# Optimization experiments

Measured on AMD Instinct MI355X. Metric: run time of the kernel, lower is better.

Reference implementation:

```python
import jax, jax.numpy as jnp
import numpy as np

N_NODES = 100000


def _gcn_conv(x, row, col, W, b, n):
    # PyG GCNConv: h = W x; out_i = sum_{j->i} norm_ij * h_j + b, with self-loops
    # and symmetric normalization norm_ij = deg_i^-1/2 * deg_j^-1/2.
    h = x @ W  # [N, out]
    loop = jnp.arange(n, dtype=row.dtype)
    r = jnp.concatenate([row, loop])
    c = jnp.concatenate([col, loop])
    deg = jax.ops.segment_sum(jnp.ones_like(c, dtype=h.dtype), c, num_segments=n)
    dinv = jnp.where(deg > 0, jax.lax.rsqrt(deg), 0.0)
    norm = dinv[r] * dinv[c]  # [E+N]
    msg = h[r] * norm[:, None]  # gather + per-edge scale
    out = jax.ops.segment_sum(msg, c, num_segments=n)  # scatter-add to dst
    return out + b


def setup_inputs() -> dict:
    key = jax.random.key(0)
    ks = jax.random.split(key, 8)
    N, E = N_NODES, 1600000
    d_in, comm_dim, hid, out = 120, 8, 128, 64
    x = jax.random.normal(ks[0], (N, d_in), dtype=jnp.float32)
    edge_index = jax.random.randint(ks[1], (2, E), 0, N, dtype=jnp.int64)
    comm_ids = jax.random.randint(ks[2], (N,), 0, 64, dtype=jnp.int64)
    comm_emb = jax.random.normal(ks[3], (64, comm_dim), dtype=jnp.float32)
    s1 = 1.0 / np.sqrt(d_in + comm_dim)
    s2 = 1.0 / np.sqrt(hid)
    W1 = jax.random.normal(ks[4], (d_in + comm_dim, hid), dtype=jnp.float32) * s1
    b1 = jnp.zeros((hid,), dtype=jnp.float32)
    W2 = jax.random.normal(ks[5], (hid, out), dtype=jnp.float32) * s2
    b2 = jnp.zeros((out,), dtype=jnp.float32)
    return {"x": x, "edge_index": edge_index, "comm_ids": comm_ids,
            "comm_emb": comm_emb, "W1": W1, "b1": b1, "W2": W2, "b2": b2}


def reference(x, edge_index, comm_ids, comm_emb, W1, b1, W2, b2):
    n = x.shape[0]
    row, col = edge_index[0], edge_index[1]
    c = comm_emb[comm_ids]                      # [N, comm_dim] embedding lookup
    h = jnp.concatenate([x, c], axis=-1)        # [N, in+comm_dim]
    h = jax.nn.relu(_gcn_conv(h, row, col, W1, b1, n))
    # dropout p=0.5 is inactive in eval mode (training=False)
    out = _gcn_conv(h, row, col, W2, b2, n)     # [N, out_channels]
    return out
```

## Files before the change

kernel.cpp:

```cpp
#include <hip/hip_runtime.h>

typedef __attribute__((ext_vector_type(8))) short bf16x8;
typedef __attribute__((ext_vector_type(4))) float f32x4;

#define CAPB 5632
#define NBMAX 512

static __device__ __forceinline__ unsigned short f2bf(float f) {
    unsigned u = __float_as_uint(f);
    unsigned r = (u + 0x7fff + ((u >> 16) & 1)) >> 16;
    return (unsigned short)r;
}
static __device__ __forceinline__ float bfu_lo(unsigned v) { return __uint_as_float(v << 16); }
static __device__ __forceinline__ float bfu_hi(unsigned v) { return __uint_as_float(v & 0xffff0000u); }
static __device__ __forceinline__ unsigned packbf(float a, float b) {
    return (unsigned)f2bf(a) | ((unsigned)f2bf(b) << 16);
}

static __device__ __forceinline__ bf16x8 cvt8(float4 u0, float4 u1) {
    bf16x8 r;
    r[0] = (short)f2bf(u0.x); r[1] = (short)f2bf(u0.y);
    r[2] = (short)f2bf(u0.z); r[3] = (short)f2bf(u0.w);
    r[4] = (short)f2bf(u1.x); r[5] = (short)f2bf(u1.y);
    r[6] = (short)f2bf(u1.z); r[7] = (short)f2bf(u1.w);
    return r;
}

__global__ void k_zero_int(int* __restrict__ p, int n) {
    int i = blockIdx.x * blockDim.x + threadIdx.x;
    if (i < n) p[i] = 0;
}

__global__ __launch_bounds__(256) void k_passA(const int* __restrict__ row,
                                               const int* __restrict__ col,
                                               int* __restrict__ gcnt,
                                               unsigned* __restrict__ packed,
                                               int E, int NB) {
    __shared__ int lcnt[NBMAX];
    __shared__ int lbase[NBMAX];
    __shared__ int lcur[NBMAX];
    __shared__ int gbaseS[NBMAX];
    __shared__ unsigned stage[4096];
    __shared__ unsigned short stageb[4096];
    __shared__ int s[256];

    int tid = threadIdx.x;
    int t0 = blockIdx.x * 4096;
    int total = min(4096, E - t0);

    for (int b = tid; b < NBMAX; b += 256) { lcnt[b] = 0; lcur[b] = 0; }
    __syncthreads();

    int er[16], ec[16];
#pragma unroll
    for (int j = 0; j < 16; ++j) {
        int e = t0 + j * 256 + tid;
        if (e < E) {
            er[j] = row[e];
            ec[j] = col[e];
            atomicAdd(&lcnt[ec[j] >> 8], 1);
        }
    }
    __syncthreads();

    int c0 = lcnt[2 * tid], c1 = lcnt[2 * tid + 1];
    int p = c0 + c1;
    s[tid] = p;
    __syncthreads();
    for (int off = 1; off < 256; off <<= 1) {
        int t = (tid >= off) ? s[tid - off] : 0;
        __syncthreads();
        s[tid] += t;
        __syncthreads();
    }
    int ebase = s[tid] - p;
    lbase[2 * tid] = ebase;
    lbase[2 * tid + 1] = ebase + c0;
    __syncthreads();

    for (int b = tid; b < NB; b += 256) {
        int lc = lcnt[b];
        if (lc > 0) gbaseS[b] = atomicAdd(&gcnt[b], lc);
    }
    __syncthreads();

#pragma unroll
    for (int j = 0; j < 16; ++j) {
        int e = t0 + j * 256 + tid;
        if (e < E) {
            int b = ec[j] >> 8;
            int pos = lbase[b] + atomicAdd(&lcur[b], 1);
            stage[pos] = ((unsigned)er[j] << 8) | ((unsigned)ec[j] & 255u);
            stageb[pos] = (unsigned short)b;
        }
    }
    __syncthreads();

    for (int j = tid; j < total; j += 256) {
        int b = stageb[j];
        packed[(size_t)b * CAPB + gbaseS[b] + (j - lbase[b])] = stage[j];
    }
}

__global__ void k_bscan(const int* __restrict__ gcnt, int* __restrict__ gbase,
                        int* __restrict__ indptr, int n, int E, int NB) {
    __shared__ int s[512];
    int tid = threadIdx.x;
    int v = (tid < NB) ? gcnt[tid] : 0;
    s[tid] = v;
    __syncthreads();
    for (int off = 1; off < 512; off <<= 1) {
        int t = (tid >= off) ? s[tid - off] : 0;
        __syncthreads();
        s[tid] += t;
        __syncthreads();
    }
    if (tid < NB) gbase[tid] = s[tid] - v;
    if (tid == 0) indptr[n] = E;
}

__global__ __launch_bounds__(256) void k_passB(const unsigned* __restrict__ packed,
                                               const int* __restrict__ gcnt,
                                               const int* __restrict__ gbase,
                                               int* __restrict__ indptr,
                                               float* __restrict__ dinv,
                                               int* __restrict__ srcidx, int n) {
    __shared__ int ncnt[256];
    __shared__ int nbase[256];
    __shared__ int srow[CAPB];

    int b = blockIdx.x;
    int tid = threadIdx.x;
    int nodeBase = b << 8;
    int cntE = min(gcnt[b], CAPB);
    int base = gbase[b];
    size_t pb = (size_t)b * CAPB;

    ncnt[tid] = 0;
    __syncthreads();

    for (int j = tid; j < cntE; j += 256) {
        unsigned e = packed[pb + j];
        atomicAdd(&ncnt[e & 255u], 1);
    }
    __syncthreads();

    int v = ncnt[tid];
    nbase[tid] = v;
    __syncthreads();
    for (int off = 1; off < 256; off <<= 1) {
        int t = (tid >= off) ? nbase[tid - off] : 0;
        __syncthreads();
        nbase[tid] += t;
        __syncthreads();
    }
    int excl = nbase[tid] - v;
    __syncthreads();
    nbase[tid] = excl;

    int node = nodeBase + tid;
    if (node < n) {
        indptr[node] = base + excl;
        dinv[node] = rsqrtf((float)(v + 1));
    }
    ncnt[tid] = 0;
    __syncthreads();

    for (int j = tid; j < cntE; j += 256) {
        unsigned e = packed[pb + j];
        int c = (int)(e & 255u);
        int r = (int)(e >> 8);
        int p = nbase[c] + atomicAdd(&ncnt[c], 1);
        srow[p] = r;
    }
    __syncthreads();

    for (int j = tid; j < cntE; j += 256) srcidx[base + j] = srow[j];
}

__global__ void k_wprep(const float* __restrict__ W1, const float* __restrict__ W2,
                        const float* __restrict__ b1,
                        unsigned short* __restrict__ Wt1, unsigned short* __restrict__ Wt2p,
                        float* __restrict__ b1p,
                        unsigned* __restrict__ D1qz,
                        unsigned* __restrict__ D2z,
                        unsigned char* __restrict__ shifts, int n) {
    int idx = blockIdx.x * blockDim.x + threadIdx.x;
    const int B0 = 128 * 128, B1 = B0 + 64 * 128, B2 = B1 + 128, B3 = B2 + 32, B4 = B3 + 32;
    if (idx < B0) {
        int colc = idx >> 7, k = idx & 127;
        Wt1[colc * 128 + k] = f2bf(W1[k * 128 + colc]);
    } else if (idx < B1) {
        int j = idx - B0;
        int colc = j >> 7, p = j & 127;
        int korig = (p & 7) * 16 + (p >> 3);
        Wt2p[colc * 128 + p] = f2bf(W2[korig * 64 + colc]);
    } else if (idx < B2) {
        int p = idx - B1;
        b1p[p] = b1[(p & 7) * 16 + (p >> 3)];
    } else if (idx < B3) {
        D1qz[idx - B2] = 0;
    } else if (idx < B4) {
        D2z[idx - B3] = 0;
    } else if (idx == B4) {
        shifts[n] = 0;
    }
}

__global__ __launch_bounds__(256) void k_gemm1(const float* __restrict__ x,
                                               const int* __restrict__ cid,
                                               const float* __restrict__ cemb,
                                               const unsigned short* __restrict__ Wt,
                                               const float* __restrict__ dinv,
                                               unsigned char* __restrict__ D1q,
                                               unsigned char* __restrict__ shifts, int n) {
    int tid = threadIdx.x;
    int wid = tid >> 6, lane = tid & 63;
    int rbase = blockIdx.x * 64 + wid * 16;
    int lr = lane & 15, kq = lane >> 4;

    int arow = rbase + lr;
    if (arow > n - 1) arow = n - 1;
    const float* xp = x + (size_t)arow * 120 + kq * 8;

    bf16x8 a0 = cvt8(*(const float4*)(xp),      *(const float4*)(xp + 4));
    bf16x8 a1 = cvt8(*(const float4*)(xp + 32), *(const float4*)(xp + 36));
    bf16x8 a2 = cvt8(*(const float4*)(xp + 64), *(const float4*)(xp + 68));
    bf16x8 a3;
    if (kq < 3) {
        a3 = cvt8(*(const float4*)(xp + 96), *(const float4*)(xp + 100));
    } else {
        const float* cp = cemb + (size_t)cid[arow] * 8;
        a3 = cvt8(*(const float4*)(cp), *(const float4*)(cp + 4));
    }

    f32x4 acc[8];
#pragma unroll
    for (int cf = 0; cf < 8; ++cf) acc[cf] = (f32x4){0.f, 0.f, 0.f, 0.f};

#pragma unroll
    for (int cf = 0; cf < 8; ++cf) {
        const unsigned short* bp = Wt + (size_t)(cf * 16 + lr) * 128 + kq * 8;
        bf16x8 b0 = *(const bf16x8*)(bp);
        bf16x8 b1 = *(const bf16x8*)(bp + 32);
        bf16x8 b2 = *(const bf16x8*)(bp + 64);
        bf16x8 b3 = *(const bf16x8*)(bp + 96);
        acc[cf] = __builtin_amdgcn_mfma_f32_16x16x32_bf16(a0, b0, acc[cf], 0, 0, 0);
        acc[cf] = __builtin_amdgcn_mfma_f32_16x16x32_bf16(a1, b1, acc[cf], 0, 0, 0);
        acc[cf] = __builtin_amdgcn_mfma_f32_16x16x32_bf16(a2, b2, acc[cf], 0, 0, 0);
        acc[cf] = __builtin_amdgcn_mfma_f32_16x16x32_bf16(a3, b3, acc[cf], 0, 0, 0);
    }

#pragma unroll
    for (int r = 0; r < 4; ++r) {
        int grow = rbase + kq * 4 + r;
        float dv = (grow < n) ? dinv[grow] : 0.f;
        float m = 0.f;
#pragma unroll
        for (int cf = 0; cf < 8; ++cf) m = fmaxf(m, fabsf(acc[cf][r] * dv));
        m = fmaxf(m, __shfl_xor(m, 1));
        m = fmaxf(m, __shfl_xor(m, 2));
        m = fmaxf(m, __shfl_xor(m, 4));
        m = fmaxf(m, __shfl_xor(m, 8));
        int mb = (int)((__float_as_uint(m) >> 23) & 255u);
        int er = mb - 127 + 1 - 7;
        int sh = min(max(er + 16, 0), 15);
        int ee = sh - 16;
        float sinv = __uint_as_float((unsigned)(127 - ee) << 23);
        if (grow < n) {
            if (lr == 0) shifts[grow] = (unsigned char)sh;
            unsigned lo = 0, hi = 0;
#pragma unroll
            for (int cf = 0; cf < 4; ++cf) {
                int q8 = (int)rintf(acc[cf][r] * dv * sinv);
                q8 = min(max(q8, -127), 127);
                lo |= ((unsigned)(q8 & 255)) << (8 * cf);
            }
#pragma unroll
            for (int cf = 4; cf < 8; ++cf) {
                int q8 = (int)rintf(acc[cf][r] * dv * sinv);
                q8 = min(max(q8, -127), 127);
                hi |= ((unsigned)(q8 & 255)) << (8 * (cf - 4));
            }
            *(uint2*)&D1q[(size_t)grow * 128 + lr * 8] = make_uint2(lo, hi);
        }
    }
}

template <int NOUT>
__global__ __launch_bounds__(256) void k_gemm_bf16(const unsigned short* __restrict__ A,
                                                   const unsigned short* __restrict__ Wt,
                                                   const float* __restrict__ dinv,
                                                   unsigned short* __restrict__ D, int n) {
    constexpr int NCF = NOUT / 16;
    int tid = threadIdx.x;
    int wid = tid >> 6, lane = tid & 63;
    int rbase = blockIdx.x * 64 + wid * 16;
    int lr = lane & 15, kq = lane >> 4;

    int arow = rbase + lr;
    if (arow > n - 1) arow = n - 1;
    const unsigned short* ap = A + (size_t)arow * 128 + kq * 8;
    bf16x8 a0 = *(const bf16x8*)(ap);
    bf16x8 a1 = *(const bf16x8*)(ap + 32);
    bf16x8 a2 = *(const bf16x8*)(ap + 64);
    bf16x8 a3 = *(const bf16x8*)(ap + 96);

    f32x4 acc[NCF];
#pragma unroll
    for (int cf = 0; cf < NCF; ++cf) acc[cf] = (f32x4){0.f, 0.f, 0.f, 0.f};

#pragma unroll
    for (int cf = 0; cf < NCF; ++cf) {
        const unsigned short* bp = Wt + (size_t)(cf * 16 + lr) * 128 + kq * 8;
        bf16x8 b0 = *(const bf16x8*)(bp);
        bf16x8 b1 = *(const bf16x8*)(bp + 32);
        bf16x8 b2 = *(const bf16x8*)(bp + 64);
        bf16x8 b3 = *(const bf16x8*)(bp + 96);
        acc[cf] = __builtin_amdgcn_mfma_f32_16x16x32_bf16(a0, b0, acc[cf], 0, 0, 0);
        acc[cf] = __builtin_amdgcn_mfma_f32_16x16x32_bf16(a1, b1, acc[cf], 0, 0, 0);
        acc[cf] = __builtin_amdgcn_mfma_f32_16x16x32_bf16(a2, b2, acc[cf], 0, 0, 0);
        acc[cf] = __builtin_amdgcn_mfma_f32_16x16x32_bf16(a3, b3, acc[cf], 0, 0, 0);
    }

    float dv[4];
#pragma unroll
    for (int r = 0; r < 4; ++r) {
        int grow = rbase + kq * 4 + r;
        dv[r] = (grow < n) ? dinv[grow] : 0.f;
    }
#pragma unroll
    for (int cf = 0; cf < NCF; ++cf) {
#pragma unroll
        for (int r = 0; r < 4; ++r) {
            int grow = rbase + kq * 4 + r;
            if (grow < n) D[(size_t)grow * NOUT + cf * 16 + lr] = f2bf(acc[cf][r] * dv[r]);
        }
    }
}

__global__ __launch_bounds__(256) void k_agg1(const uint2* __restrict__ rows,
                                              const unsigned char* __restrict__ shifts,
                                              const int* __restrict__ indptr,
                                              const int* __restrict__ srcidx,
                                              const float* __restrict__ dinv,
                                              const float* __restrict__ b1p,
                                              uint4* __restrict__ Out, int n) {
    int tid = threadIdx.x;
    int lane = tid & 63;
    int g = lane >> 4, gl = lane & 15;
    int i = blockIdx.x * 16 + (tid >> 6) * 4 + g;
    if (i > n - 1) i = n - 1;

    float di = dinv[i];
    float4 bA = *(const float4*)&b1p[gl * 8];
    float4 bB = *(const float4*)&b1p[gl * 8 + 4];

    uint2 sq = rows[(size_t)i * 16 + gl];
    int ssh = shifts[i];
    int a[8];
#pragma unroll
    for (int j = 0; j < 4; ++j) {
        a[j]     = ((int)(signed char)((sq.x >> (8 * j)) & 255u)) << ssh;
        a[j + 4] = ((int)(signed char)((sq.y >> (8 * j)) & 255u)) << ssh;
    }

    int e0 = indptr[i];
    int d = indptr[i + 1] - e0;
    int m = max(d, __shfl_xor(d, 16));
    m = max(m, __shfl_xor(m, 32));

#pragma unroll 4
    for (int t = 0; t < m; ++t) {
        bool act = t < d;
        int s = act ? srcidx[e0 + t] : n;
        int sh = shifts[s];
        uint2 q = rows[(size_t)s * 16 + gl];
#pragma unroll
        for (int j = 0; j < 4; ++j) {
            a[j]     += ((int)(signed char)((q.x >> (8 * j)) & 255u)) << sh;
            a[j + 4] += ((int)(signed char)((q.y >> (8 * j)) & 255u)) << sh;
        }
    }

    float sc = di * 0x1p-16f;
    uint4 o;
    o.x = packbf(fmaxf((float)a[0] * sc + bA.x, 0.f), fmaxf((float)a[1] * sc + bA.y, 0.f));
    o.y = packbf(fmaxf((float)a[2] * sc + bA.z, 0.f), fmaxf((float)a[3] * sc + bA.w, 0.f));
    o.z = packbf(fmaxf((float)a[4] * sc + bB.x, 0.f), fmaxf((float)a[5] * sc + bB.y, 0.f));
    o.w = packbf(fmaxf((float)a[6] * sc + bB.z, 0.f), fmaxf((float)a[7] * sc + bB.w, 0.f));
    Out[(size_t)i * 16 + gl] = o;
}

__global__ __launch_bounds__(256) void k_agg2(const uint2* __restrict__ Hs,
                                              const int* __restrict__ indptr,
                                              const int* __restrict__ srcidx,
                                              const float* __restrict__ dinv,
                                              const float* __restrict__ bias,
                                              float4* __restrict__ Out, int n) {
    int tid = threadIdx.x;
    int lane = tid & 63;
    int g = lane >> 4, gl = lane & 15;
    int i = blockIdx.x * 16 + (tid >> 6) * 4 + g;
    if (i > n - 1) i = n - 1;

    float di = dinv[i];
    float4 b = *(const float4*)&bias[gl * 4];

    uint2 sv = Hs[(size_t)i * 16 + gl];
    float a0 = bfu_lo(sv.x), a1 = bfu_hi(sv.x);
    float a2 = bfu_lo(sv.y), a3 = bfu_hi(sv.y);

    int e0 = indptr[i];
    int d = indptr[i + 1] - e0;
    int m = max(d, __shfl_xor(d, 16));
    m = max(m, __shfl_xor(m, 32));

#pragma unroll 4
    for (int t = 0; t < m; ++t) {
        bool act = t < d;
        int s = act ? srcidx[e0 + t] : n;
        uint2 w = Hs[(size_t)s * 16 + gl];
        a0 += bfu_lo(w.x);
        a1 += bfu_hi(w.x);
        a2 += bfu_lo(w.y);
        a3 += bfu_hi(w.y);
    }
    Out[(size_t)i * 16 + gl] = make_float4(di * a0 + b.x, di * a1 + b.y,
                                           di * a2 + b.z, di * a3 + b.w);
}


extern "C" void kernel_launch(void* const* d_in, const int* in_sizes, int n_in,
                              void* d_out, int out_size, void* d_ws, size_t ws_size,
                              hipStream_t stream) {
    const float* x    = (const float*)d_in[0];
    const int*   eidx = (const int*)d_in[1];
    const int*   cid  = (const int*)d_in[2];
    const float* cemb = (const float*)d_in[3];
    const float* W1   = (const float*)d_in[4];
    const float* b1   = (const float*)d_in[5];
    const float* W2   = (const float*)d_in[6];
    const float* b2   = (const float*)d_in[7];
    float* out = (float*)d_out;

    int n = in_sizes[2];
    int E = in_sizes[1] / 2;
    const int* row = eidx;
    const int* col = eidx + E;
    int NB = (n + 255) / 256;

    char* ws = (char*)d_ws;
    auto alloc = [&](size_t bytes) {
        char* p = ws;
        ws += (bytes + 255) & ~(size_t)255;
        return p;
    };
    float*          dinv   = (float*)alloc((size_t)n * 4);
    int*            gcnt   = (int*)alloc((size_t)NB * 4);
    int*            gbase  = (int*)alloc((size_t)NB * 4);
    int*            indptr = (int*)alloc((size_t)(n + 1) * 4);
    int*            srcidx = (int*)alloc((size_t)E * 4);
    unsigned*       packed = (unsigned*)alloc((size_t)NB * CAPB * 4);
    unsigned short* Wt1    = (unsigned short*)alloc(128 * 128 * 2);
    unsigned short* Wt2p   = (unsigned short*)alloc(64 * 128 * 2);
    float*          b1p    = (float*)alloc(128 * 4);
    unsigned char*  D1q    = (unsigned char*)alloc((size_t)(n + 1) * 128);
    unsigned char*  shifts = (unsigned char*)alloc((size_t)(n + 1));
    unsigned short* H1p    = (unsigned short*)alloc((size_t)n * 128 * 2);
    unsigned short* D2     = (unsigned short*)alloc((size_t)(n + 1) * 64 * 2);

    k_zero_int<<<(NB + 255) / 256, 256, 0, stream>>>(gcnt, NB);
    k_passA<<<(E + 4095) / 4096, 256, 0, stream>>>(row, col, gcnt, packed, E, NB);
    k_bscan<<<1, 512, 0, stream>>>(gcnt, gbase, indptr, n, E, NB);
    k_passB<<<NB, 256, 0, stream>>>(packed, gcnt, gbase, indptr, dinv, srcidx, n);

    int wpn = 128 * 128 + 64 * 128 + 128 + 32 + 32 + 1;
    k_wprep<<<(wpn + 255) / 256, 256, 0, stream>>>(
        W1, W2, b1, Wt1, Wt2p, b1p,
        (unsigned*)(D1q + (size_t)n * 128),
        (unsigned*)(D2 + (size_t)n * 64),
        shifts, n);

    int gb = (n + 63) / 64;
    int ga = (n + 15) / 16;
    k_gemm1<<<gb, 256, 0, stream>>>(x, cid, cemb, Wt1, dinv, D1q, shifts, n);
    k_agg1<<<ga, 256, 0, stream>>>((const uint2*)D1q, shifts, indptr, srcidx, dinv, b1p,
                                   (uint4*)H1p, n);
    k_gemm_bf16<64><<<gb, 256, 0, stream>>>(H1p, Wt2p, dinv, D2, n);
    k_agg2<<<ga, 256, 0, stream>>>((const uint2*)D2, indptr, srcidx, dinv, b2,
                                   (float4*)out, n);
}
```

Baseline: 197.2 us.

## Sort nodes by in-degree to balance wavefront work in aggregation kernels

```diff
diff --git a/kernel.cpp b/kernel.cpp
--- a/kernel.cpp
+++ b/kernel.cpp
@@ -103,7 +103,8 @@
 }
 
 __global__ void k_bscan(const int* __restrict__ gcnt, int* __restrict__ gbase,
-                        int* __restrict__ indptr, int n, int E, int NB) {
+                        int* __restrict__ indptr, int* __restrict__ hist,
+                        int n, int E, int NB) {
     __shared__ int s[512];
     int tid = threadIdx.x;
     int v = (tid < NB) ? gcnt[tid] : 0;
@@ -117,6 +118,7 @@
     }
     if (tid < NB) gbase[tid] = s[tid] - v;
     if (tid == 0) indptr[n] = E;
+    if (tid < 64) hist[tid] = 0;
 }
 
 __global__ __launch_bounds__(256) void k_passB(const unsigned* __restrict__ packed,
@@ -176,6 +178,57 @@
     __syncthreads();
 
     for (int j = tid; j < cntE; j += 256) srcidx[base + j] = srow[j];
+}
+
+__global__ void k_hist(const int* __restrict__ indptr, int* __restrict__ hist, int n) {
+    __shared__ int lh[64];
+    int tid = threadIdx.x;
+    if (tid < 64) lh[tid] = 0;
+    __syncthreads();
+    int i = blockIdx.x * 256 + tid;
+    if (i < n) {
+        int d = min(indptr[i + 1] - indptr[i], 63);
+        atomicAdd(&lh[d], 1);
+    }
+    __syncthreads();
+    if (tid < 64 && lh[tid]) atomicAdd(&hist[tid], lh[tid]);
+}
+
+__global__ void k_hscan(int* __restrict__ hist, int* __restrict__ dbase) {
+    __shared__ int s[64];
+    int t = threadIdx.x;
+    int v = hist[t];
+    s[t] = v;
+    __syncthreads();
+    for (int off = 1; off < 64; off <<= 1) {
+        int u = (t >= off) ? s[t - off] : 0;
+        __syncthreads();
+        s[t] += u;
+        __syncthreads();
+    }
+    dbase[t] = s[t] - v;
+    hist[t] = 0;
+}
+
+__global__ void k_dscatter(const int* __restrict__ indptr, const int* __restrict__ dbase,
+                           int* __restrict__ gcur, int* __restrict__ nodeord, int n) {
+    __shared__ int lh[64], lbase[64], lcur[64];
+    int t = threadIdx.x;
+    if (t < 64) { lh[t] = 0; lcur[t] = 0; }
+    __syncthreads();
+    int i = blockIdx.x * 256 + t;
+    int d = -1;
+    if (i < n) {
+        d = min(indptr[i + 1] - indptr[i], 63);
+        atomicAdd(&lh[d], 1);
+    }
+    __syncthreads();
+    if (t < 64 && lh[t]) lbase[t] = atomicAdd(&gcur[t], lh[t]);
+    __syncthreads();
+    if (i < n) {
+        int r = atomicAdd(&lcur[d], 1);
+        nodeord[dbase[d] + lbase[d] + r] = i;
+    }
 }
 
 __global__ void k_wprep(const float* __restrict__ W1, const float* __restrict__ W2,
@@ -343,14 +396,16 @@
                                               const unsigned char* __restrict__ shifts,
                                               const int* __restrict__ indptr,
                                               const int* __restrict__ srcidx,
+                                              const int* __restrict__ nodeord,
                                               const float* __restrict__ dinv,
                                               const float* __restrict__ b1p,
                                               uint4* __restrict__ Out, int n) {
     int tid = threadIdx.x;
     int lane = tid & 63;
     int g = lane >> 4, gl = lane & 15;
-    int i = blockIdx.x * 16 + (tid >> 6) * 4 + g;
-    if (i > n - 1) i = n - 1;
+    int slot = blockIdx.x * 16 + (tid >> 6) * 4 + g;
+    if (slot > n - 1) slot = n - 1;
+    int i = nodeord[slot];
 
     float di = dinv[i];
     float4 bA = *(const float4*)&b1p[gl * 8];
@@ -370,7 +425,7 @@
     int m = max(d, __shfl_xor(d, 16));
     m = max(m, __shfl_xor(m, 32));
 
-#pragma unroll 4
+#pragma unroll 8
     for (int t = 0; t < m; ++t) {
         bool act = t < d;
         int s = act ? srcidx[e0 + t] : n;
@@ -395,14 +450,16 @@
 __global__ __launch_bounds__(256) void k_agg2(const uint2* __restrict__ Hs,
                                               const int* __restrict__ indptr,
                                               const int* __restrict__ srcidx,
+                                              const int* __restrict__ nodeord,
                                               const float* __restrict__ dinv,
                                               const float* __restrict__ bias,
                                               float4* __restrict__ Out, int n) {
     int tid = threadIdx.x;
     int lane = tid & 63;
     int g = lane >> 4, gl = lane & 15;
-    int i = blockIdx.x * 16 + (tid >> 6) * 4 + g;
-    if (i > n - 1) i = n - 1;
+    int slot = blockIdx.x * 16 + (tid >> 6) * 4 + g;
+    if (slot > n - 1) slot = n - 1;
+    int i = nodeord[slot];
 
     float di = dinv[i];
     float4 b = *(const float4*)&bias[gl * 4];
@@ -416,7 +473,7 @@
     int m = max(d, __shfl_xor(d, 16));
     m = max(m, __shfl_xor(m, 32));
 
-#pragma unroll 4
+#pragma unroll 8
     for (int t = 0; t < m; ++t) {
         bool act = t < d;
         int s = act ? srcidx[e0 + t] : n;
@@ -456,24 +513,31 @@
         ws += (bytes + 255) & ~(size_t)255;
         return p;
     };
-    float*          dinv   = (float*)alloc((size_t)n * 4);
-    int*            gcnt   = (int*)alloc((size_t)NB * 4);
-    int*            gbase  = (int*)alloc((size_t)NB * 4);
-    int*            indptr = (int*)alloc((size_t)(n + 1) * 4);
-    int*            srcidx = (int*)alloc((size_t)E * 4);
-    unsigned*       packed = (unsigned*)alloc((size_t)NB * CAPB * 4);
-    unsigned short* Wt1    = (unsigned short*)alloc(128 * 128 * 2);
-    unsigned short* Wt2p   = (unsigned short*)alloc(64 * 128 * 2);
-    float*          b1p    = (float*)alloc(128 * 4);
-    unsigned char*  D1q    = (unsigned char*)alloc((size_t)(n + 1) * 128);
-    unsigned char*  shifts = (unsigned char*)alloc((size_t)(n + 1));
-    unsigned short* H1p    = (unsigned short*)alloc((size_t)n * 128 * 2);
-    unsigned short* D2     = (unsigned short*)alloc((size_t)(n + 1) * 64 * 2);
+    float*          dinv    = (float*)alloc((size_t)n * 4);
+    int*            gcnt    = (int*)alloc((size_t)NB * 4);
+    int*            gbase   = (int*)alloc((size_t)NB * 4);
+    int*            indptr  = (int*)alloc((size_t)(n + 1) * 4);
+    int*            srcidx  = (int*)alloc((size_t)E * 4);
+    unsigned*       packed  = (unsigned*)alloc((size_t)NB * CAPB * 4);
+    int*            hist    = (int*)alloc(64 * 4);
+    int*            dbase   = (int*)alloc(64 * 4);
+    int*            nodeord = (int*)alloc((size_t)n * 4);
+    unsigned short* Wt1     = (unsigned short*)alloc(128 * 128 * 2);
+    unsigned short* Wt2p    = (unsigned short*)alloc(64 * 128 * 2);
+    float*          b1p     = (float*)alloc(128 * 4);
+    unsigned char*  D1q     = (unsigned char*)alloc((size_t)(n + 1) * 128);
+    unsigned char*  shifts  = (unsigned char*)alloc((size_t)(n + 1));
+    unsigned short* H1p     = (unsigned short*)alloc((size_t)n * 128 * 2);
+    unsigned short* D2      = (unsigned short*)alloc((size_t)(n + 1) * 64 * 2);
 
     k_zero_int<<<(NB + 255) / 256, 256, 0, stream>>>(gcnt, NB);
     k_passA<<<(E + 4095) / 4096, 256, 0, stream>>>(row, col, gcnt, packed, E, NB);
-    k_bscan<<<1, 512, 0, stream>>>(gcnt, gbase, indptr, n, E, NB);
+    k_bscan<<<1, 512, 0, stream>>>(gcnt, gbase, indptr, hist, n, E, NB);
     k_passB<<<NB, 256, 0, stream>>>(packed, gcnt, gbase, indptr, dinv, srcidx, n);
+
+    k_hist<<<NB, 256, 0, stream>>>(indptr, hist, n);
+    k_hscan<<<1, 64, 0, stream>>>(hist, dbase);
+    k_dscatter<<<NB, 256, 0, stream>>>(indptr, dbase, hist, nodeord, n);
 
     int wpn = 128 * 128 + 64 * 128 + 128 + 32 + 32 + 1;
     k_wprep<<<(wpn + 255) / 256, 256, 0, stream>>>(
@@ -485,9 +549,9 @@
     int gb = (n + 63) / 64;
     int ga = (n + 15) / 16;
     k_gemm1<<<gb, 256, 0, stream>>>(x, cid, cemb, Wt1, dinv, D1q, shifts, n);
-    k_agg1<<<ga, 256, 0, stream>>>((const uint2*)D1q, shifts, indptr, srcidx, dinv, b1p,
-                                   (uint4*)H1p, n);
+    k_agg1<<<ga, 256, 0, stream>>>((const uint2*)D1q, shifts, indptr, srcidx, nodeord,
+                                   dinv, b1p, (uint4*)H1p, n);
     k_gemm_bf16<64><<<gb, 256, 0, stream>>>(H1p, Wt2p, dinv, D2, n);
-    k_agg2<<<ga, 256, 0, stream>>>((const uint2*)D2, indptr, srcidx, dinv, b2,
+    k_agg2<<<ga, 256, 0, stream>>>((const uint2*)D2, indptr, srcidx, nodeord, dinv, b2,
                                    (float4*)out, n);
 }
```

After: 208.4 us. 1.06x slower.

## Fuse layer-1 aggregation with layer-2 GEMM via shared-memory tile

Applied to the files above, without the earlier changes.

```diff
diff --git a/kernel.cpp b/kernel.cpp
--- a/kernel.cpp
+++ b/kernel.cpp
@@ -13,9 +13,6 @@
 }
 static __device__ __forceinline__ float bfu_lo(unsigned v) { return __uint_as_float(v << 16); }
 static __device__ __forceinline__ float bfu_hi(unsigned v) { return __uint_as_float(v & 0xffff0000u); }
-static __device__ __forceinline__ unsigned packbf(float a, float b) {
-    return (unsigned)f2bf(a) | ((unsigned)f2bf(b) << 16);
-}
 
 static __device__ __forceinline__ bf16x8 cvt8(float4 u0, float4 u1) {
     bf16x8 r;
@@ -287,69 +284,19 @@
     }
 }
 
-template <int NOUT>
-__global__ __launch_bounds__(256) void k_gemm_bf16(const unsigned short* __restrict__ A,
-                                                   const unsigned short* __restrict__ Wt,
-                                                   const float* __restrict__ dinv,
-                                                   unsigned short* __restrict__ D, int n) {
-    constexpr int NCF = NOUT / 16;
+__global__ __launch_bounds__(256) void k_agg1g2(const uint2* __restrict__ rows,
+                                                const unsigned char* __restrict__ shifts,
+                                                const int* __restrict__ indptr,
+                                                const int* __restrict__ srcidx,
+                                                const float* __restrict__ dinv,
+                                                const float* __restrict__ b1p,
+                                                const unsigned short* __restrict__ Wt2p,
+                                                unsigned short* __restrict__ D2, int n) {
+    __shared__ unsigned short Hl[16][132];
     int tid = threadIdx.x;
     int wid = tid >> 6, lane = tid & 63;
-    int rbase = blockIdx.x * 64 + wid * 16;
-    int lr = lane & 15, kq = lane >> 4;
-
-    int arow = rbase + lr;
-    if (arow > n - 1) arow = n - 1;
-    const unsigned short* ap = A + (size_t)arow * 128 + kq * 8;
-    bf16x8 a0 = *(const bf16x8*)(ap);
-    bf16x8 a1 = *(const bf16x8*)(ap + 32);
-    bf16x8 a2 = *(const bf16x8*)(ap + 64);
-    bf16x8 a3 = *(const bf16x8*)(ap + 96);
-
-    f32x4 acc[NCF];
-#pragma unroll
-    for (int cf = 0; cf < NCF; ++cf) acc[cf] = (f32x4){0.f, 0.f, 0.f, 0.f};
-
-#pragma unroll
-    for (int cf = 0; cf < NCF; ++cf) {
-        const unsigned short* bp = Wt + (size_t)(cf * 16 + lr) * 128 + kq * 8;
-        bf16x8 b0 = *(const bf16x8*)(bp);
-        bf16x8 b1 = *(const bf16x8*)(bp + 32);
-        bf16x8 b2 = *(const bf16x8*)(bp + 64);
-        bf16x8 b3 = *(const bf16x8*)(bp + 96);
-        acc[cf] = __builtin_amdgcn_mfma_f32_16x16x32_bf16(a0, b0, acc[cf], 0, 0, 0);
-        acc[cf] = __builtin_amdgcn_mfma_f32_16x16x32_bf16(a1, b1, acc[cf], 0, 0, 0);
-        acc[cf] = __builtin_amdgcn_mfma_f32_16x16x32_bf16(a2, b2, acc[cf], 0, 0, 0);
-        acc[cf] = __builtin_amdgcn_mfma_f32_16x16x32_bf16(a3, b3, acc[cf], 0, 0, 0);
-    }
-
-    float dv[4];
-#pragma unroll
-    for (int r = 0; r < 4; ++r) {
-        int grow = rbase + kq * 4 + r;
-        dv[r] = (grow < n) ? dinv[grow] : 0.f;
-    }
-#pragma unroll
-    for (int cf = 0; cf < NCF; ++cf) {
-#pragma unroll
-        for (int r = 0; r < 4; ++r) {
-            int grow = rbase + kq * 4 + r;
-            if (grow < n) D[(size_t)grow * NOUT + cf * 16 + lr] = f2bf(acc[cf][r] * dv[r]);
-        }
-    }
-}
-
-__global__ __launch_bounds__(256) void k_agg1(const uint2* __restrict__ rows,
-                                              const unsigned char* __restrict__ shifts,
-                                              const int* __restrict__ indptr,
-                                              const int* __restrict__ srcidx,
-                                              const float* __restrict__ dinv,
-                                              const float* __restrict__ b1p,
-                                              uint4* __restrict__ Out, int n) {
-    int tid = threadIdx.x;
-    int lane = tid & 63;
     int g = lane >> 4, gl = lane & 15;
-    int i = blockIdx.x * 16 + (tid >> 6) * 4 + g;
+    int i = blockIdx.x * 16 + wid * 4 + g;
     if (i > n - 1) i = n - 1;
 
     float di = dinv[i];
@@ -370,7 +317,7 @@
     int m = max(d, __shfl_xor(d, 16));
     m = max(m, __shfl_xor(m, 32));
 
-#pragma unroll 4
+#pragma unroll 8
     for (int t = 0; t < m; ++t) {
         bool act = t < d;
         int s = act ? srcidx[e0 + t] : n;
@@ -384,12 +331,30 @@
     }
 
     float sc = di * 0x1p-16f;
-    uint4 o;
-    o.x = packbf(fmaxf((float)a[0] * sc + bA.x, 0.f), fmaxf((float)a[1] * sc + bA.y, 0.f));
-    o.y = packbf(fmaxf((float)a[2] * sc + bA.z, 0.f), fmaxf((float)a[3] * sc + bA.w, 0.f));
-    o.z = packbf(fmaxf((float)a[4] * sc + bB.x, 0.f), fmaxf((float)a[5] * sc + bB.y, 0.f));
-    o.w = packbf(fmaxf((float)a[6] * sc + bB.z, 0.f), fmaxf((float)a[7] * sc + bB.w, 0.f));
-    Out[(size_t)i * 16 + gl] = o;
+    int trow = wid * 4 + g;
+    float hb[8] = {bA.x, bA.y, bA.z, bA.w, bB.x, bB.y, bB.z, bB.w};
+#pragma unroll
+    for (int j = 0; j < 8; ++j) {
+        Hl[trow][gl * 8 + j] = f2bf(fmaxf((float)a[j] * sc + hb[j], 0.f));
+    }
+    __syncthreads();
+
+    int lr = lane & 15, kq = lane >> 4;
+    f32x4 acc = (f32x4){0.f, 0.f, 0.f, 0.f};
+    const unsigned short* bp = Wt2p + (size_t)(wid * 16 + lr) * 128 + kq * 8;
+#pragma unroll
+    for (int step = 0; step < 4; ++step) {
+        bf16x8 af = *(const bf16x8*)&Hl[lr][kq * 8 + step * 32];
+        bf16x8 bf = *(const bf16x8*)(bp + step * 32);
+        acc = __builtin_amdgcn_mfma_f32_16x16x32_bf16(af, bf, acc, 0, 0, 0);
+    }
+#pragma unroll
+    for (int r = 0; r < 4; ++r) {
+        int node = blockIdx.x * 16 + kq * 4 + r;
+        if (node < n) {
+            D2[(size_t)node * 64 + wid * 16 + lr] = f2bf(acc[r] * dinv[node]);
+        }
+    }
 }
 
 __global__ __launch_bounds__(256) void k_agg2(const uint2* __restrict__ Hs,
@@ -416,7 +381,7 @@
     int m = max(d, __shfl_xor(d, 16));
     m = max(m, __shfl_xor(m, 32));
 
-#pragma unroll 4
+#pragma unroll 8
     for (int t = 0; t < m; ++t) {
         bool act = t < d;
         int s = act ? srcidx[e0 + t] : n;
@@ -456,19 +421,18 @@
         ws += (bytes + 255) & ~(size_t)255;
         return p;
     };
-    float*          dinv   = (float*)alloc((size_t)n * 4);
-    int*            gcnt   = (int*)alloc((size_t)NB * 4);
-    int*            gbase  = (int*)alloc((size_t)NB * 4);
-    int*            indptr = (int*)alloc((size_t)(n + 1) * 4);
-    int*            srcidx = (int*)alloc((size_t)E * 4);
-    unsigned*       packed = (unsigned*)alloc((size_t)NB * CAPB * 4);
-    unsigned short* Wt1    = (unsigned short*)alloc(128 * 128 * 2);
-    unsigned short* Wt2p   = (unsigned short*)alloc(64 * 128 * 2);
-    float*          b1p    = (float*)alloc(128 * 4);
-    unsigned char*  D1q    = (unsigned char*)alloc((size_t)(n + 1) * 128);
-    unsigned char*  shifts = (unsigned char*)alloc((size_t)(n + 1));
-    unsigned short* H1p    = (unsigned short*)alloc((size_t)n * 128 * 2);
-    unsigned short* D2     = (unsigned short*)alloc((size_t)(n + 1) * 64 * 2);
+    float*          dinv    = (float*)alloc((size_t)n * 4);
+    int*            gcnt    = (int*)alloc((size_t)NB * 4);
+    int*            gbase   = (int*)alloc((size_t)NB * 4);
+    int*            indptr  = (int*)alloc((size_t)(n + 1) * 4);
+    int*            srcidx  = (int*)alloc((size_t)E * 4);
+    unsigned*       packed  = (unsigned*)alloc((size_t)NB * CAPB * 4);
+    unsigned short* Wt1     = (unsigned short*)alloc(128 * 128 * 2);
+    unsigned short* Wt2p    = (unsigned short*)alloc(64 * 128 * 2);
+    float*          b1p     = (float*)alloc(128 * 4);
+    unsigned char*  D1q     = (unsigned char*)alloc((size_t)(n + 1) * 128);
+    unsigned char*  shifts  = (unsigned char*)alloc((size_t)(n + 1));
+    unsigned short* D2      = (unsigned short*)alloc((size_t)(n + 1) * 64 * 2);
 
     k_zero_int<<<(NB + 255) / 256, 256, 0, stream>>>(gcnt, NB);
     k_passA<<<(E + 4095) / 4096, 256, 0, stream>>>(row, col, gcnt, packed, E, NB);
@@ -485,9 +449,8 @@
     int gb = (n + 63) / 64;
     int ga = (n + 15) / 16;
     k_gemm1<<<gb, 256, 0, stream>>>(x, cid, cemb, Wt1, dinv, D1q, shifts, n);
-    k_agg1<<<ga, 256, 0, stream>>>((const uint2*)D1q, shifts, indptr, srcidx, dinv, b1p,
-                                   (uint4*)H1p, n);
-    k_gemm_bf16<64><<<gb, 256, 0, stream>>>(H1p, Wt2p, dinv, D2, n);
+    k_agg1g2<<<ga, 256, 0, stream>>>((const uint2*)D1q, shifts, indptr, srcidx,
+                                     dinv, b1p, Wt2p, D2, n);
     k_agg2<<<ga, 256, 0, stream>>>((const uint2*)D2, indptr, srcidx, dinv, b2,
                                    (float4*)out, n);
 }
```

Measured after the change: 188.5 us. -4.4%, faster.
